# Kernel tuning notes

Measured on AMD Instinct MI355X. Metric: run time of the kernel, lower is better.

Reference implementation:

```python
import jax, jax.numpy as jnp
import numpy as np
import math

SEQ, BATCH, H, E, V = 2048, 64, 512, 256, 50257


def _gru_cell(x, h, W_ih, W_hh, b_ih, b_hh):
    # PyTorch GRU cell: gates ordered (r, z, n)
    gi = x @ W_ih.T + b_ih            # [B, 3H]
    gh = h @ W_hh.T + b_hh            # [B, 3H]
    i_r, i_z, i_n = jnp.split(gi, 3, axis=1)
    h_r, h_z, h_n = jnp.split(gh, 3, axis=1)
    r = jax.nn.sigmoid(i_r + h_r)
    z = jax.nn.sigmoid(i_z + h_z)
    n = jnp.tanh(i_n + r * h_n)
    return (1.0 - z) * n + z * h


def setup_inputs() -> dict:
    key = jax.random.key(0)
    ks = jax.random.split(key, 14)
    s = 1.0 / math.sqrt(H)
    inp = {
        "inputs": jax.random.randint(ks[0], (BATCH,), 0, V),
        "dec_hidden": jax.random.normal(ks[1], (2, BATCH, H), jnp.float32),
        "enc_outputs": jax.random.normal(ks[2], (SEQ, BATCH, H), jnp.float32),
        "emb": jax.random.normal(ks[3], (V, E), jnp.float32),
        # layer 0: input dim = H + E
        "W_ih0": jax.random.uniform(ks[4], (3 * H, H + E), jnp.float32, -s, s),
        "W_hh0": jax.random.uniform(ks[5], (3 * H, H), jnp.float32, -s, s),
        "b_ih0": jax.random.uniform(ks[6], (3 * H,), jnp.float32, -s, s),
        "b_hh0": jax.random.uniform(ks[7], (3 * H,), jnp.float32, -s, s),
        # layer 1: input dim = H
        "W_ih1": jax.random.uniform(ks[8], (3 * H, H), jnp.float32, -s, s),
        "W_hh1": jax.random.uniform(ks[9], (3 * H, H), jnp.float32, -s, s),
        "b_ih1": jax.random.uniform(ks[10], (3 * H,), jnp.float32, -s, s),
        "b_hh1": jax.random.uniform(ks[11], (3 * H,), jnp.float32, -s, s),
        "out_W": jax.random.uniform(ks[12], (V, H), jnp.float32, -s, s),
        "out_b": jax.random.uniform(ks[13], (V,), jnp.float32, -s, s),
    }
    return inp


def reference(inputs, dec_hidden, enc_outputs, emb,
              W_ih0, W_hh0, b_ih0, b_hh0,
              W_ih1, W_hh1, b_ih1, b_hh1,
              out_W, out_b):
    # --- dot-product attention (vectorized over seq) ---
    h_top = dec_hidden[-1]                                     # [B, H]
    scale = 1.0 / math.sqrt(H)
    energy = jnp.einsum('bh,sbh->sb', h_top, enc_outputs) * scale  # [S, B]
    alpha = jax.nn.softmax(energy, axis=0)                     # softmax over seq
    context = jnp.einsum('sb,sbh->bh', alpha, enc_outputs)     # [B, H]
    # --- embed + concat ---
    embeddings = emb[inputs]                                   # [B, E]
    x = jnp.concatenate([embeddings, context], axis=1)         # [B, E+H]
    # --- 2-layer GRU, single time step (eval mode: no dropout) ---
    h0 = _gru_cell(x, dec_hidden[0], W_ih0, W_hh0, b_ih0, b_hh0)
    h1 = _gru_cell(h0, dec_hidden[1], W_ih1, W_hh1, b_ih1, b_hh1)
    new_hidden = jnp.stack([h0, h1], axis=0)                   # [2, B, H]
    # --- vocab projection ---
    logits = h1 @ out_W.T + out_b                              # [B, V]
    return logits, new_hidden
```

## Files before the change

### kernel.cpp

```cpp
#include <hip/hip_runtime.h>
#include <math.h>

#define SEQ   2048
#define BATCH 64
#define HDIM  512
#define EDIM  256
#define VOCAB 50257
#define BH    (BATCH * HDIM)
#define G3    (3 * HDIM)
#define NCOL  (2 * G3)

typedef __attribute__((ext_vector_type(4))) float f32x4;
typedef __attribute__((ext_vector_type(8))) short bf16x8;

__device__ __forceinline__ unsigned short f2bf(float x) {
    unsigned int u = __float_as_uint(x);
    u += 0x7fffu + ((u >> 16) & 1u);
    return (unsigned short)(u >> 16);
}

__device__ __forceinline__ bf16x8 pack8(float4 a, float4 b) {
    bf16x8 r;
    r[0] = (short)f2bf(a.x); r[1] = (short)f2bf(a.y);
    r[2] = (short)f2bf(a.z); r[3] = (short)f2bf(a.w);
    r[4] = (short)f2bf(b.x); r[5] = (short)f2bf(b.y);
    r[6] = (short)f2bf(b.z); r[7] = (short)f2bf(b.w);
    return r;
}

__device__ __forceinline__ bf16x8 cvt8(const float* p) {
    return pack8(*(const float4*)p, *(const float4*)(p + 4));
}

__global__ __launch_bounds__(256)
void attn_partial(const float* __restrict__ enc, const float* __restrict__ dec,
                  float* __restrict__ pm, float* __restrict__ pl,
                  float* __restrict__ pacc, int P, int rows) {
    const int lane = threadIdx.x & 63;
    const int wave = threadIdx.x >> 6;
    const int p = blockIdx.x * 4 + wave;
    const int b = blockIdx.y;
    const int s0 = p * rows;
    const float scale = 0.044194173824159216f;

    const float4* qp = (const float4*)(dec + BH + (size_t)b * HDIM + 8 * lane);
    float4 q0 = qp[0], q1 = qp[1];
    float qa[8] = {q0.x, q0.y, q0.z, q0.w, q1.x, q1.y, q1.z, q1.w};

    float m = -INFINITY, l = 0.f;
    float acc[8] = {0.f, 0.f, 0.f, 0.f, 0.f, 0.f, 0.f, 0.f};

    #pragma unroll 2
    for (int r = 0; r < rows; r += 4) {
        float va[4][8];
        #pragma unroll
        for (int j = 0; j < 4; ++j) {
            const float4* vp = (const float4*)(enc +
                ((size_t)(s0 + r + j) * BATCH + b) * HDIM + 8 * lane);
            float4 t0 = vp[0], t1 = vp[1];
            va[j][0] = t0.x; va[j][1] = t0.y; va[j][2] = t0.z; va[j][3] = t0.w;
            va[j][4] = t1.x; va[j][5] = t1.y; va[j][6] = t1.z; va[j][7] = t1.w;
        }
        float e[4];
        #pragma unroll
        for (int j = 0; j < 4; ++j) {
            float d = 0.f;
            #pragma unroll
            for (int i = 0; i < 8; ++i) d = fmaf(va[j][i], qa[i], d);
            e[j] = d;
        }
        #pragma unroll
        for (int off = 32; off > 0; off >>= 1) {
            #pragma unroll
            for (int j = 0; j < 4; ++j) e[j] += __shfl_xor(e[j], off, 64);
        }
        #pragma unroll
        for (int j = 0; j < 4; ++j) e[j] *= scale;
        float m4 = fmaxf(fmaxf(e[0], e[1]), fmaxf(e[2], e[3]));
        float em = fmaxf(m, m4);
        float f  = __expf(m - em);
        float w0 = __expf(e[0] - em), w1 = __expf(e[1] - em);
        float w2 = __expf(e[2] - em), w3 = __expf(e[3] - em);
        l = l * f + (w0 + w1 + w2 + w3);
        #pragma unroll
        for (int i = 0; i < 8; ++i) {
            float a = acc[i] * f;
            a = fmaf(w0, va[0][i], a);
            a = fmaf(w1, va[1][i], a);
            a = fmaf(w2, va[2][i], a);
            acc[i] = fmaf(w3, va[3][i], a);
        }
        m = em;
    }

    float* pa = pacc + ((size_t)b * P + p) * HDIM + 8 * lane;
    #pragma unroll
    for (int i = 0; i < 8; ++i) pa[i] = acc[i];
    if (lane == 0) { pm[b * P + p] = m; pl[b * P + p] = l; }
}

__global__ __launch_bounds__(512)
void attn_combine(const float* __restrict__ pm, const float* __restrict__ pl,
                  const float* __restrict__ pacc, const float* __restrict__ dec,
                  const float* __restrict__ emb, const int* __restrict__ inputs,
                  unsigned short* __restrict__ xbf,
                  unsigned short* __restrict__ d0bf,
                  unsigned short* __restrict__ d1bf, int P) {
    __shared__ float s_coef[128];
    __shared__ float s_inv;
    const int b = blockIdx.x;
    const int t = threadIdx.x;

    if (t < 64) {
        float mloc = -INFINITY;
        for (int p = t; p < P; p += 64) mloc = fmaxf(mloc, pm[b * P + p]);
        #pragma unroll
        for (int off = 32; off > 0; off >>= 1) mloc = fmaxf(mloc, __shfl_xor(mloc, off, 64));
        float d = 0.f;
        for (int p = t; p < P; p += 64) {
            float c = __expf(pm[b * P + p] - mloc);
            s_coef[p] = c;
            d = fmaf(c, pl[b * P + p], d);
        }
        #pragma unroll
        for (int off = 32; off > 0; off >>= 1) d += __shfl_xor(d, off, 64);
        if (t == 0) s_inv = 1.f / d;
    }
    __syncthreads();

    float c = 0.f;
    const float* pa = pacc + (size_t)b * P * HDIM + t;
    #pragma unroll 4
    for (int p = 0; p < P; ++p) c = fmaf(s_coef[p], pa[(size_t)p * HDIM], c);
    float ctx = c * s_inv;

    xbf[(size_t)b * (EDIM + HDIM) + EDIM + t] = f2bf(ctx);
    if (t < EDIM)
        xbf[(size_t)b * (EDIM + HDIM) + t] = f2bf(emb[(size_t)inputs[b] * EDIM + t]);
    d0bf[(size_t)b * HDIM + t] = f2bf(dec[(size_t)b * HDIM + t]);
    d1bf[(size_t)b * HDIM + t] = f2bf(dec[BH + (size_t)b * HDIM + t]);
}

template<int K1>
__global__ __launch_bounds__(256)
void gru_gemm(const unsigned short* __restrict__ Aih,
              const unsigned short* __restrict__ Ahh,
              const float* __restrict__ Wih,
              const float* __restrict__ Whh,
              float* __restrict__ part) {
    const int lane = threadIdx.x & 63;
    const int nt = blockIdx.x * 4 + (threadIdx.x >> 6);
    const int kc = blockIdx.y;
    const int nn = lane & 15;
    const int koff = (lane >> 4) * 8;

    const bool ih = nt < 96;
    const int col16 = ih ? nt : nt - 96;
    const int g = col16 * 16 + nn;
    const int K = ih ? K1 : HDIM;
    const int kchunk = K >> 1;
    const int k0 = kc * kchunk;

    const float* wrow = (ih ? Wih : Whh) + (size_t)g * K + k0 + koff;
    const unsigned short* arow = (ih ? Aih : Ahh) + (size_t)nn * K + k0 + koff;

    f32x4 acc[4];
    #pragma unroll
    for (int mt = 0; mt < 4; ++mt) acc[mt] = (f32x4){0, 0, 0, 0};

    const int nks = kchunk >> 5;
    #pragma unroll 4
    for (int ks = 0; ks < nks; ++ks) {
        bf16x8 bf = cvt8(wrow + 32 * ks);
        #pragma unroll
        for (int mt = 0; mt < 4; ++mt) {
            bf16x8 a = *(const bf16x8*)(arow + (size_t)mt * 16 * K + 32 * ks);
            acc[mt] = __builtin_amdgcn_mfma_f32_16x16x32_bf16(a, bf, acc[mt], 0, 0, 0);
        }
    }

    const int col = col16 * 16 + nn + (ih ? 0 : G3);
    float* pp = part + ((size_t)kc * NCOL + col) * 64 + (lane >> 4) * 4;
    #pragma unroll
    for (int mt = 0; mt < 4; ++mt)
        *(f32x4*)(pp + mt * 16) = acc[mt];
}

__global__ __launch_bounds__(256)
void gru_gate(const float* __restrict__ part,
              const float* __restrict__ hprev,
              const float* __restrict__ bih, const float* __restrict__ bhh,
              float* __restrict__ hout, unsigned short* __restrict__ houtBf) {
    const int gidx = blockIdx.x * 256 + threadIdx.x;
    const int b = gidx & 63;
    const int h = gidx >> 6;

    #define PRD(c) (part[(size_t)(c) * 64 + b] + part[(size_t)((c) + NCOL) * 64 + b])
    float ir = PRD(h),            hr = PRD(G3 + h);
    float iz = PRD(HDIM + h),     hz = PRD(G3 + HDIM + h);
    float in_ = PRD(2 * HDIM + h), hn = PRD(G3 + 2 * HDIM + h);
    #undef PRD

    float r = 1.f / (1.f + __expf(-(ir + bih[h] + hr + bhh[h])));
    float z = 1.f / (1.f + __expf(-(iz + bih[HDIM + h] + hz + bhh[HDIM + h])));
    float n = tanhf(in_ + bih[2 * HDIM + h] + r * (hn + bhh[2 * HDIM + h]));
    float hp = hprev[(size_t)b * HDIM + h];
    float hnew = (1.f - z) * n + z * hp;

    hout[(size_t)b * HDIM + h] = hnew;
    houtBf[(size_t)b * HDIM + h] = f2bf(hnew);
}

__global__ __launch_bounds__(256)
void vocab_proj_mfma(const unsigned short* __restrict__ h1bf,
                     const float* __restrict__ Wout,
                     const float* __restrict__ bout,
                     float* __restrict__ logits) {
    const int NPAIR = (VOCAB + 31) / 32;
    const int lane = threadIdx.x & 63;
    const int w = blockIdx.x * 4 + (threadIdx.x >> 6);
    if (w >= NPAIR) return;

    const int nn = lane & 15;
    const int koff = (lane >> 4) * 8;
    const int vA = w * 32 + nn;
    const int vB = vA + 16;
    const int vAc = min(vA, VOCAB - 1);
    const int vBc = min(vB, VOCAB - 1);

    const float* wrowA = Wout + (size_t)vAc * HDIM + koff;
    const float* wrowB = Wout + (size_t)vBc * HDIM + koff;
    const unsigned short* arow = h1bf + nn * HDIM + koff;

    f32x4 accA[4], accB[4];
    #pragma unroll
    for (int mt = 0; mt < 4; ++mt) { accA[mt] = (f32x4){0,0,0,0}; accB[mt] = (f32x4){0,0,0,0}; }

    float4 pa0 = *(const float4*)(wrowA);
    float4 pa1 = *(const float4*)(wrowA + 4);
    float4 pb0 = *(const float4*)(wrowB);
    float4 pb1 = *(const float4*)(wrowB + 4);

    #pragma unroll
    for (int ks = 0; ks < 16; ++ks) {
        float4 ca0 = pa0, ca1 = pa1, cb0 = pb0, cb1 = pb1;
        if (ks < 15) {
            pa0 = *(const float4*)(wrowA + 32 * (ks + 1));
            pa1 = *(const float4*)(wrowA + 32 * (ks + 1) + 4);
            pb0 = *(const float4*)(wrowB + 32 * (ks + 1));
            pb1 = *(const float4*)(wrowB + 32 * (ks + 1) + 4);
        }
        bf16x8 bA = pack8(ca0, ca1);
        bf16x8 bB = pack8(cb0, cb1);
        #pragma unroll
        for (int mt = 0; mt < 4; ++mt) {
            bf16x8 a = *(const bf16x8*)(arow + (size_t)mt * 16 * HDIM + 32 * ks);
            accA[mt] = __builtin_amdgcn_mfma_f32_16x16x32_bf16(a, bA, accA[mt], 0, 0, 0);
            accB[mt] = __builtin_amdgcn_mfma_f32_16x16x32_bf16(a, bB, accB[mt], 0, 0, 0);
        }
    }

    const int b0 = (lane >> 4) * 4;
    if (vA < VOCAB) {
        const float bias = bout[vA];
        #pragma unroll
        for (int mt = 0; mt < 4; ++mt)
            #pragma unroll
            for (int r = 0; r < 4; ++r)
                logits[(size_t)(mt * 16 + b0 + r) * VOCAB + vA] = accA[mt][r] + bias;
    }
    if (vB < VOCAB) {
        const float bias = bout[vB];
        #pragma unroll
        for (int mt = 0; mt < 4; ++mt)
            #pragma unroll
            for (int r = 0; r < 4; ++r)
                logits[(size_t)(mt * 16 + b0 + r) * VOCAB + vB] = accB[mt][r] + bias;
    }
}

extern "C" void kernel_launch(void* const* d_in, const int* in_sizes, int n_in,
                              void* d_out, int out_size, void* d_ws, size_t ws_size,
                              hipStream_t stream) {
    const int*   inputs = (const int*)d_in[0];
    const float* dec    = (const float*)d_in[1];
    const float* enc    = (const float*)d_in[2];
    const float* emb    = (const float*)d_in[3];
    const float* Wih0   = (const float*)d_in[4];
    const float* Whh0   = (const float*)d_in[5];
    const float* bih0   = (const float*)d_in[6];
    const float* bhh0   = (const float*)d_in[7];
    const float* Wih1   = (const float*)d_in[8];
    const float* Whh1   = (const float*)d_in[9];
    const float* bih1   = (const float*)d_in[10];
    const float* bhh1   = (const float*)d_in[11];
    const float* Wout   = (const float*)d_in[12];
    const float* bout   = (const float*)d_in[13];
    float* out = (float*)d_out;

    int P = 128;
    while (P > 4) {
        size_t need = ((size_t)P * BATCH * (HDIM + 2) + 2u * NCOL * 64) * sizeof(float)
                      + 2u * (BATCH * (EDIM + HDIM) + 4u * BH);
        if (need <= ws_size) break;
        P >>= 1;
    }
    const int rows = SEQ / P;

    float* w    = (float*)d_ws;
    float* pm   = w;
    float* pl   = pm + (size_t)P * BATCH;
    float* pacc = pl + (size_t)P * BATCH;
    float* part = pacc + (size_t)P * BATCH * HDIM;
    unsigned short* xbf  = (unsigned short*)(part + 2 * (size_t)NCOL * 64);
    unsigned short* d0bf = xbf + (size_t)BATCH * (EDIM + HDIM);
    unsigned short* d1bf = d0bf + BH;
    unsigned short* h0bf = d1bf + BH;
    unsigned short* h1bf = h0bf + BH;

    float* h0out = out + (size_t)BATCH * VOCAB;
    float* h1out = h0out + BH;

    attn_partial<<<dim3(P / 4, BATCH), 256, 0, stream>>>(enc, dec, pm, pl, pacc, P, rows);
    attn_combine<<<BATCH, 512, 0, stream>>>(pm, pl, pacc, dec, emb, inputs, xbf, d0bf, d1bf, P);

    gru_gemm<EDIM + HDIM><<<dim3(48, 2), 256, 0, stream>>>(xbf, d0bf, Wih0, Whh0, part);
    gru_gate<<<128, 256, 0, stream>>>(part, dec, bih0, bhh0, h0out, h0bf);
    gru_gemm<HDIM><<<dim3(48, 2), 256, 0, stream>>>(h0bf, d1bf, Wih1, Whh1, part);
    gru_gate<<<128, 256, 0, stream>>>(part, dec + BH, bih1, bhh1, h1out, h1bf);

    const int NPAIR = (VOCAB + 31) / 32;
    vocab_proj_mfma<<<(NPAIR + 3) / 4, 256, 0, stream>>>(h1bf, Wout, bout, out);
}
```

Measured before the change: 142.8 us.

## Merge attention partials in-block, split GRU K four ways, one vocab tile per wave

The attention partial kernel now fixes 32 blocks per batch. Its four waves each handle 16 rows and merge their online-softmax state in shared memory before writing, which shrinks the partial buffers the combine kernel has to read. The GRU GEMMs split K into four chunks instead of two, giving twice as many blocks, and the gate kernel now sums four partials. The vocab projection gives each wave a single 16-column tile with a 3-deep prefetch ring of weight loads, doubling the wave count but lowering register use. The workspace-size fallback loop is removed, so the code assumes the workspace is large enough.

```diff
diff --git a/kernel.cpp b/kernel.cpp
--- a/kernel.cpp
+++ b/kernel.cpp
@@ -9,6 +9,8 @@
 #define BH    (BATCH * HDIM)
 #define G3    (3 * HDIM)
 #define NCOL  (2 * G3)
+#define P32   32
+#define KS    4
 
 typedef __attribute__((ext_vector_type(4))) float f32x4;
 typedef __attribute__((ext_vector_type(8))) short bf16x8;
@@ -35,12 +37,12 @@
 __global__ __launch_bounds__(256)
 void attn_partial(const float* __restrict__ enc, const float* __restrict__ dec,
                   float* __restrict__ pm, float* __restrict__ pl,
-                  float* __restrict__ pacc, int P, int rows) {
+                  float* __restrict__ pacc) {
     const int lane = threadIdx.x & 63;
-    const int wave = threadIdx.x >> 6;
-    const int p = blockIdx.x * 4 + wave;
+    const int w = threadIdx.x >> 6;
+    const int p = blockIdx.x;
     const int b = blockIdx.y;
-    const int s0 = p * rows;
+    const int s0 = (p * 4 + w) * 16;
     const float scale = 0.044194173824159216f;
 
     const float4* qp = (const float4*)(dec + BH + (size_t)b * HDIM + 8 * lane);
@@ -51,7 +53,7 @@
     float acc[8] = {0.f, 0.f, 0.f, 0.f, 0.f, 0.f, 0.f, 0.f};
 
     #pragma unroll 2
-    for (int r = 0; r < rows; r += 4) {
+    for (int r = 0; r < 16; r += 4) {
         float va[4][8];
         #pragma unroll
         for (int j = 0; j < 4; ++j) {
@@ -93,10 +95,29 @@
         m = em;
     }
 
-    float* pa = pacc + ((size_t)b * P + p) * HDIM + 8 * lane;
-    #pragma unroll
-    for (int i = 0; i < 8; ++i) pa[i] = acc[i];
-    if (lane == 0) { pm[b * P + p] = m; pl[b * P + p] = l; }
+    __shared__ float sacc[4][HDIM];
+    __shared__ float sml[8];
+    #pragma unroll
+    for (int i = 0; i < 8; ++i) sacc[w][8 * lane + i] = acc[i];
+    if (lane == 0) { sml[w] = m; sml[4 + w] = l; }
+    __syncthreads();
+
+    const float m0 = sml[0], m1 = sml[1], m2 = sml[2], m3 = sml[3];
+    const float ms = fmaxf(fmaxf(m0, m1), fmaxf(m2, m3));
+    const float c0 = __expf(m0 - ms), c1 = __expf(m1 - ms);
+    const float c2 = __expf(m2 - ms), c3 = __expf(m3 - ms);
+    const int t = threadIdx.x;
+    #pragma unroll
+    for (int i = 0; i < 2; ++i) {
+        const int h = t + i * 256;
+        float v = c0 * sacc[0][h] + c1 * sacc[1][h]
+                + c2 * sacc[2][h] + c3 * sacc[3][h];
+        pacc[((size_t)b * P32 + p) * HDIM + h] = v;
+    }
+    if (t == 0) {
+        pm[b * P32 + p] = ms;
+        pl[b * P32 + p] = c0 * sml[4] + c1 * sml[5] + c2 * sml[6] + c3 * sml[7];
+    }
 }
 
 __global__ __launch_bounds__(512)
@@ -105,22 +126,22 @@
                   const float* __restrict__ emb, const int* __restrict__ inputs,
                   unsigned short* __restrict__ xbf,
                   unsigned short* __restrict__ d0bf,
-                  unsigned short* __restrict__ d1bf, int P) {
-    __shared__ float s_coef[128];
+                  unsigned short* __restrict__ d1bf) {
+    __shared__ float s_coef[P32];
     __shared__ float s_inv;
     const int b = blockIdx.x;
     const int t = threadIdx.x;
 
     if (t < 64) {
         float mloc = -INFINITY;
-        for (int p = t; p < P; p += 64) mloc = fmaxf(mloc, pm[b * P + p]);
+        for (int p = t; p < P32; p += 64) mloc = fmaxf(mloc, pm[b * P32 + p]);
         #pragma unroll
         for (int off = 32; off > 0; off >>= 1) mloc = fmaxf(mloc, __shfl_xor(mloc, off, 64));
         float d = 0.f;
-        for (int p = t; p < P; p += 64) {
-            float c = __expf(pm[b * P + p] - mloc);
+        for (int p = t; p < P32; p += 64) {
+            float c = __expf(pm[b * P32 + p] - mloc);
             s_coef[p] = c;
-            d = fmaf(c, pl[b * P + p], d);
+            d = fmaf(c, pl[b * P32 + p], d);
         }
         #pragma unroll
         for (int off = 32; off > 0; off >>= 1) d += __shfl_xor(d, off, 64);
@@ -129,9 +150,9 @@
     __syncthreads();
 
     float c = 0.f;
-    const float* pa = pacc + (size_t)b * P * HDIM + t;
-    #pragma unroll 4
-    for (int p = 0; p < P; ++p) c = fmaf(s_coef[p], pa[(size_t)p * HDIM], c);
+    const float* pa = pacc + (size_t)b * P32 * HDIM + t;
+    #pragma unroll 8
+    for (int p = 0; p < P32; ++p) c = fmaf(s_coef[p], pa[(size_t)p * HDIM], c);
     float ctx = c * s_inv;
 
     xbf[(size_t)b * (EDIM + HDIM) + EDIM + t] = f2bf(ctx);
@@ -158,7 +179,7 @@
     const int col16 = ih ? nt : nt - 96;
     const int g = col16 * 16 + nn;
     const int K = ih ? K1 : HDIM;
-    const int kchunk = K >> 1;
+    const int kchunk = K >> 2;
     const int k0 = kc * kchunk;
 
     const float* wrow = (ih ? Wih : Whh) + (size_t)g * K + k0 + koff;
@@ -169,7 +190,7 @@
     for (int mt = 0; mt < 4; ++mt) acc[mt] = (f32x4){0, 0, 0, 0};
 
     const int nks = kchunk >> 5;
-    #pragma unroll 4
+    #pragma unroll 2
     for (int ks = 0; ks < nks; ++ks) {
         bf16x8 bf = cvt8(wrow + 32 * ks);
         #pragma unroll
@@ -195,9 +216,12 @@
     const int b = gidx & 63;
     const int h = gidx >> 6;
 
-    #define PRD(c) (part[(size_t)(c) * 64 + b] + part[(size_t)((c) + NCOL) * 64 + b])
-    float ir = PRD(h),            hr = PRD(G3 + h);
-    float iz = PRD(HDIM + h),     hz = PRD(G3 + HDIM + h);
+    #define PRD(c) (part[(size_t)(c) * 64 + b] \
+                  + part[((size_t)NCOL + (c)) * 64 + b] \
+                  + part[((size_t)2 * NCOL + (c)) * 64 + b] \
+                  + part[((size_t)3 * NCOL + (c)) * 64 + b])
+    float ir = PRD(h),             hr = PRD(G3 + h);
+    float iz = PRD(HDIM + h),      hz = PRD(G3 + HDIM + h);
     float in_ = PRD(2 * HDIM + h), hn = PRD(G3 + 2 * HDIM + h);
     #undef PRD
 
@@ -216,66 +240,53 @@
                      const float* __restrict__ Wout,
                      const float* __restrict__ bout,
                      float* __restrict__ logits) {
-    const int NPAIR = (VOCAB + 31) / 32;
+    const int NT = (VOCAB + 15) / 16;
     const int lane = threadIdx.x & 63;
-    const int w = blockIdx.x * 4 + (threadIdx.x >> 6);
-    if (w >= NPAIR) return;
+    const int nt = blockIdx.x * 4 + (threadIdx.x >> 6);
+    if (nt >= NT) return;
 
     const int nn = lane & 15;
+    const int v  = nt * 16 + nn;
+    const int vclamp = min(v, VOCAB - 1);
     const int koff = (lane >> 4) * 8;
-    const int vA = w * 32 + nn;
-    const int vB = vA + 16;
-    const int vAc = min(vA, VOCAB - 1);
-    const int vBc = min(vB, VOCAB - 1);
-
-    const float* wrowA = Wout + (size_t)vAc * HDIM + koff;
-    const float* wrowB = Wout + (size_t)vBc * HDIM + koff;
+
+    const float* wrow = Wout + (size_t)vclamp * HDIM + koff;
     const unsigned short* arow = h1bf + nn * HDIM + koff;
 
-    f32x4 accA[4], accB[4];
-    #pragma unroll
-    for (int mt = 0; mt < 4; ++mt) { accA[mt] = (f32x4){0,0,0,0}; accB[mt] = (f32x4){0,0,0,0}; }
-
-    float4 pa0 = *(const float4*)(wrowA);
-    float4 pa1 = *(const float4*)(wrowA + 4);
-    float4 pb0 = *(const float4*)(wrowB);
-    float4 pb1 = *(const float4*)(wrowB + 4);
+    f32x4 acc[4];
+    #pragma unroll
+    for (int mt = 0; mt < 4; ++mt) acc[mt] = (f32x4){0, 0, 0, 0};
+
+    float4 pw0[3], pw1[3];
+    #pragma unroll
+    for (int d = 0; d < 3; ++d) {
+        pw0[d] = *(const float4*)(wrow + 32 * d);
+        pw1[d] = *(const float4*)(wrow + 32 * d + 4);
+    }
 
     #pragma unroll
     for (int ks = 0; ks < 16; ++ks) {
-        float4 ca0 = pa0, ca1 = pa1, cb0 = pb0, cb1 = pb1;
-        if (ks < 15) {
-            pa0 = *(const float4*)(wrowA + 32 * (ks + 1));
-            pa1 = *(const float4*)(wrowA + 32 * (ks + 1) + 4);
-            pb0 = *(const float4*)(wrowB + 32 * (ks + 1));
-            pb1 = *(const float4*)(wrowB + 32 * (ks + 1) + 4);
-        }
-        bf16x8 bA = pack8(ca0, ca1);
-        bf16x8 bB = pack8(cb0, cb1);
+        const int slot = ks % 3;
+        bf16x8 bfrag = pack8(pw0[slot], pw1[slot]);
+        if (ks + 3 < 16) {
+            pw0[slot] = *(const float4*)(wrow + 32 * (ks + 3));
+            pw1[slot] = *(const float4*)(wrow + 32 * (ks + 3) + 4);
+        }
         #pragma unroll
         for (int mt = 0; mt < 4; ++mt) {
             bf16x8 a = *(const bf16x8*)(arow + (size_t)mt * 16 * HDIM + 32 * ks);
-            accA[mt] = __builtin_amdgcn_mfma_f32_16x16x32_bf16(a, bA, accA[mt], 0, 0, 0);
-            accB[mt] = __builtin_amdgcn_mfma_f32_16x16x32_bf16(a, bB, accB[mt], 0, 0, 0);
-        }
-    }
-
-    const int b0 = (lane >> 4) * 4;
-    if (vA < VOCAB) {
-        const float bias = bout[vA];
+            acc[mt] = __builtin_amdgcn_mfma_f32_16x16x32_bf16(a, bfrag, acc[mt], 0, 0, 0);
+        }
+    }
+
+    if (v < VOCAB) {
+        const float bias = bout[v];
+        const int b0 = (lane >> 4) * 4;
         #pragma unroll
         for (int mt = 0; mt < 4; ++mt)
             #pragma unroll
             for (int r = 0; r < 4; ++r)
-                logits[(size_t)(mt * 16 + b0 + r) * VOCAB + vA] = accA[mt][r] + bias;
-    }
-    if (vB < VOCAB) {
-        const float bias = bout[vB];
-        #pragma unroll
-        for (int mt = 0; mt < 4; ++mt)
-            #pragma unroll
-            for (int r = 0; r < 4; ++r)
-                logits[(size_t)(mt * 16 + b0 + r) * VOCAB + vB] = accB[mt][r] + bias;
+                logits[(size_t)(mt * 16 + b0 + r) * VOCAB + v] = acc[mt][r] + bias;
     }
 }
 
@@ -298,21 +309,12 @@
     const float* bout   = (const float*)d_in[13];
     float* out = (float*)d_out;
 
-    int P = 128;
-    while (P > 4) {
-        size_t need = ((size_t)P * BATCH * (HDIM + 2) + 2u * NCOL * 64) * sizeof(float)
-                      + 2u * (BATCH * (EDIM + HDIM) + 4u * BH);
-        if (need <= ws_size) break;
-        P >>= 1;
-    }
-    const int rows = SEQ / P;
-
     float* w    = (float*)d_ws;
     float* pm   = w;
-    float* pl   = pm + (size_t)P * BATCH;
-    float* pacc = pl + (size_t)P * BATCH;
-    float* part = pacc + (size_t)P * BATCH * HDIM;
-    unsigned short* xbf  = (unsigned short*)(part + 2 * (size_t)NCOL * 64);
+    float* pl   = pm + (size_t)P32 * BATCH;
+    float* pacc = pl + (size_t)P32 * BATCH;
+    float* part = pacc + (size_t)P32 * BATCH * HDIM;
+    unsigned short* xbf  = (unsigned short*)(part + (size_t)KS * NCOL * 64);
     unsigned short* d0bf = xbf + (size_t)BATCH * (EDIM + HDIM);
     unsigned short* d1bf = d0bf + BH;
     unsigned short* h0bf = d1bf + BH;
@@ -321,14 +323,14 @@
     float* h0out = out + (size_t)BATCH * VOCAB;
     float* h1out = h0out + BH;
 
-    attn_partial<<<dim3(P / 4, BATCH), 256, 0, stream>>>(enc, dec, pm, pl, pacc, P, rows);
-    attn_combine<<<BATCH, 512, 0, stream>>>(pm, pl, pacc, dec, emb, inputs, xbf, d0bf, d1bf, P);
-
-    gru_gemm<EDIM + HDIM><<<dim3(48, 2), 256, 0, stream>>>(xbf, d0bf, Wih0, Whh0, part);
+    attn_partial<<<dim3(P32, BATCH), 256, 0, stream>>>(enc, dec, pm, pl, pacc);
+    attn_combine<<<BATCH, 512, 0, stream>>>(pm, pl, pacc, dec, emb, inputs, xbf, d0bf, d1bf);
+
+    gru_gemm<EDIM + HDIM><<<dim3(48, KS), 256, 0, stream>>>(xbf, d0bf, Wih0, Whh0, part);
     gru_gate<<<128, 256, 0, stream>>>(part, dec, bih0, bhh0, h0out, h0bf);
-    gru_gemm<HDIM><<<dim3(48, 2), 256, 0, stream>>>(h0bf, d1bf, Wih1, Whh1, part);
+    gru_gemm<HDIM><<<dim3(48, KS), 256, 0, stream>>>(h0bf, d1bf, Wih1, Whh1, part);
     gru_gate<<<128, 256, 0, stream>>>(part, dec + BH, bih1, bhh1, h1out, h1bf);
 
-    const int NPAIR = (VOCAB + 31) / 32;
-    vocab_proj_mfma<<<(NPAIR + 3) / 4, 256, 0, stream>>>(h1bf, Wout, bout, out);
-}
+    const int NT = (VOCAB + 15) / 16;
+    vocab_proj_mfma<<<(NT + 3) / 4, 256, 0, stream>>>(h1bf, Wout, bout, out);
+}
```

Result: faster. 140.0 us (-2.0%).
